# Kernel tuning notes

Hardware: AMD Instinct MI355X
Metric: run time of the kernel (lower is better)

The kernel has to match this reference:

```python
import jax, jax.numpy as jnp
import numpy as np

INVALID_VALUE = 0.0
FIX_SEARCH_AREA = 1  # search window half-width -> (2s+1)^2 candidates


def setup_inputs() -> dict:
    key = jax.random.key(0)
    k1, k2, k3 = jax.random.split(key, 3)
    B, C, H, W = 8, 1, 512, 512
    Ho, Wo = 1024, 1024
    depth = jax.random.uniform(k1, (B, C, H, W), dtype=jnp.float32, minval=0.5, maxval=5.0)
    holes = jax.random.uniform(k2, (B, C, H, W)) < 0.25
    depth = jnp.where(holes, INVALID_VALUE, depth)
    # normalized grid coords in [-1.2, 1.2]: some samples out of bounds (Zeros padding)
    grid = jax.random.uniform(k3, (B, Ho, Wo, 2), dtype=jnp.float32, minval=-1.2, maxval=1.2)
    return {"input": depth, "grid": grid}


def _search_offsets(s):
    # center offset first, then ring offsets in row-major order
    offs = [(0, 0)] + [(dy, dx) for dy in range(-s, s + 1) for dx in range(-s, s + 1)
                       if not (dy == 0 and dx == 0)]
    dys = jnp.array([o[0] for o in offs], dtype=jnp.int32)
    dxs = jnp.array([o[1] for o in offs], dtype=jnp.int32)
    return dys, dxs


def reference(input, grid):
    """MaskPlusFix nearest sampling with local search-area fix, Zeros padding,
    align_corners=True. input: (B,C,H,W), grid: (B,Ho,Wo,2) -> (B,C,Ho,Wo)."""
    B, C, H, W = input.shape
    # unnormalize (align_corners=True): [-1,1] -> [0, size-1]
    x = (grid[..., 0] + 1.0) * 0.5 * (W - 1)
    y = (grid[..., 1] + 1.0) * 0.5 * (H - 1)
    ix = jnp.round(x).astype(jnp.int32)  # nearest pixel (B,Ho,Wo)
    iy = jnp.round(y).astype(jnp.int32)

    dys, dxs = _search_offsets(FIX_SEARCH_AREA)  # (K,)
    cix = ix[..., None] + dxs  # (B,Ho,Wo,K)
    ciy = iy[..., None] + dys
    inb = (cix >= 0) & (cix < W) & (ciy >= 0) & (ciy < H)  # Zeros padding: OOB invalid
    cixc = jnp.clip(cix, 0, W - 1)
    ciyc = jnp.clip(ciy, 0, H - 1)

    # gather candidates: (B,C,Ho,Wo,K)
    vals = jax.vmap(lambda img, yy, xx: img[:, yy, xx])(input, ciyc, cixc)
    valid = inb[:, None] & (vals != INVALID_VALUE)
    first = jnp.argmax(valid, axis=-1)
    any_valid = jnp.any(valid, axis=-1)
    sel = jnp.take_along_axis(vals, first[..., None], axis=-1)[..., 0]
    return jnp.where(any_valid, sel, INVALID_VALUE)
```

## Files before the change

kernel.cpp:

```cpp
#include <hip/hip_runtime.h>


#define SC_B  8
#define SC_H  512
#define SC_W  512
#define SC_HO 1024
#define SC_WO 1024

__global__ __launch_bounds__(256) void SpaceCarverGridSamplerModule_kernel(
    const float* __restrict__ depth,
    const float* __restrict__ grid,
    float* __restrict__ out,
    int total)
{
    int idx = blockIdx.x * blockDim.x + threadIdx.x;
    if (idx >= total) return;

    int b = idx >> 20;

    float2 g = reinterpret_cast<const float2*>(grid)[idx];

    float x = (g.x + 1.0f) * 0.5f * (float)(SC_W - 1);
    float y = (g.y + 1.0f) * 0.5f * (float)(SC_H - 1);

    int ix = (int)rintf(x);
    int iy = (int)rintf(y);

    const float* __restrict__ img = depth + (size_t)b * (SC_H * SC_W);

    const int dys[9] = { 0, -1, -1, -1,  0, 0,  1, 1, 1 };
    const int dxs[9] = { 0, -1,  0,  1, -1, 1, -1, 0, 1 };

    float result = 0.0f;
    #pragma unroll
    for (int k = 0; k < 9; ++k) {
        int cy = iy + dys[k];
        int cx = ix + dxs[k];
        if (cy >= 0 && cy < SC_H && cx >= 0 && cx < SC_W) {
            float v = img[cy * SC_W + cx];
            if (v != 0.0f) { result = v; break; }
        }
    }

    out[idx] = result;
}

extern "C" void kernel_launch(void* const* d_in, const int* in_sizes, int n_in,
                              void* d_out, int out_size, void* d_ws, size_t ws_size,
                              hipStream_t stream) {
    const float* depth = (const float*)d_in[0];
    const float* grid  = (const float*)d_in[1];
    float* out = (float*)d_out;

    int total = out_size;
    dim3 block(256);
    dim3 gridDim((total + block.x - 1) / block.x);
    SpaceCarverGridSamplerModule_kernel<<<gridDim, block, 0, stream>>>(depth, grid, out, total);
}
```

Baseline: 144.6 us.

## Process two samples per thread and issue all nine gathers unconditionally

```diff
diff --git a/kernel.cpp b/kernel.cpp
--- a/kernel.cpp
+++ b/kernel.cpp
@@ -7,42 +7,59 @@
 #define SC_HO 1024
 #define SC_WO 1024
 
+__device__ __forceinline__ float sample_one(const float* __restrict__ img,
+                                            float gx, float gy)
+{
+    float x = (gx + 1.0f) * 0.5f * (float)(SC_W - 1);
+    float y = (gy + 1.0f) * 0.5f * (float)(SC_H - 1);
+
+    int ix = (int)rintf(x);
+    int iy = (int)rintf(y);
+
+    const int dys[9] = { 0, -1, -1, -1,  0, 0,  1, 1, 1 };
+    const int dxs[9] = { 0, -1,  0,  1, -1, 1, -1, 0, 1 };
+
+    float v[9];
+    bool  inb[9];
+    #pragma unroll
+    for (int k = 0; k < 9; ++k) {
+        int cy = iy + dys[k];
+        int cx = ix + dxs[k];
+        inb[k] = (cy >= 0) & (cy < SC_H) & (cx >= 0) & (cx < SC_W);
+        int cyc = min(max(cy, 0), SC_H - 1);
+        int cxc = min(max(cx, 0), SC_W - 1);
+        v[k] = img[cyc * SC_W + cxc];
+    }
+
+    float result = 0.0f;
+    #pragma unroll
+    for (int k = 8; k >= 0; --k) {
+        bool valid = inb[k] & (v[k] != 0.0f);
+        result = valid ? v[k] : result;
+    }
+    return result;
+}
+
 __global__ __launch_bounds__(256) void SpaceCarverGridSamplerModule_kernel(
     const float* __restrict__ depth,
     const float* __restrict__ grid,
     float* __restrict__ out,
-    int total)
+    int total_pairs)
 {
-    int idx = blockIdx.x * blockDim.x + threadIdx.x;
-    if (idx >= total) return;
+    int t = blockIdx.x * blockDim.x + threadIdx.x;
+    if (t >= total_pairs) return;
 
-    int b = idx >> 20;
+    int idx0 = t * 2;
+    int b = idx0 >> 20;
 
-    float2 g = reinterpret_cast<const float2*>(grid)[idx];
-
-    float x = (g.x + 1.0f) * 0.5f * (float)(SC_W - 1);
-    float y = (g.y + 1.0f) * 0.5f * (float)(SC_H - 1);
-
-    int ix = (int)rintf(x);
-    int iy = (int)rintf(y);
+    float4 g = reinterpret_cast<const float4*>(grid)[t];
 
     const float* __restrict__ img = depth + (size_t)b * (SC_H * SC_W);
 
-    const int dys[9] = { 0, -1, -1, -1,  0, 0,  1, 1, 1 };
-    const int dxs[9] = { 0, -1,  0,  1, -1, 1, -1, 0, 1 };
+    float r0 = sample_one(img, g.x, g.y);
+    float r1 = sample_one(img, g.z, g.w);
 
-    float result = 0.0f;
-    #pragma unroll
-    for (int k = 0; k < 9; ++k) {
-        int cy = iy + dys[k];
-        int cx = ix + dxs[k];
-        if (cy >= 0 && cy < SC_H && cx >= 0 && cx < SC_W) {
-            float v = img[cy * SC_W + cx];
-            if (v != 0.0f) { result = v; break; }
-        }
-    }
-
-    out[idx] = result;
+    reinterpret_cast<float2*>(out)[t] = make_float2(r0, r1);
 }
 
 extern "C" void kernel_launch(void* const* d_in, const int* in_sizes, int n_in,
@@ -52,8 +69,8 @@
     const float* grid  = (const float*)d_in[1];
     float* out = (float*)d_out;
 
-    int total = out_size;
+    int total_pairs = out_size / 2;
     dim3 block(256);
-    dim3 gridDim((total + block.x - 1) / block.x);
-    SpaceCarverGridSamplerModule_kernel<<<gridDim, block, 0, stream>>>(depth, grid, out, total);
+    dim3 gridDim((total_pairs + block.x - 1) / block.x);
+    SpaceCarverGridSamplerModule_kernel<<<gridDim, block, 0, stream>>>(depth, grid, out, total_pairs);
 }
```

After: 219.0 us. 51.4% more time.

## Precompute fixed depth map in padded buffer, then single-gather sampling

Applied to the files above, without the earlier changes.

```diff
diff --git a/kernel.cpp b/kernel.cpp
--- a/kernel.cpp
+++ b/kernel.cpp
@@ -7,7 +7,92 @@
 #define SC_HO 1024
 #define SC_WO 1024
 
-__global__ __launch_bounds__(256) void SpaceCarverGridSamplerModule_kernel(
+#define FP_H  514
+#define FP_W  514
+#define FP_S  516
+#define FP_BATCH (FP_H * FP_S)
+
+__global__ __launch_bounds__(256) void build_fixed_kernel(
+    const float* __restrict__ depth,
+    float* __restrict__ fixedPad)
+{
+    int b = blockIdx.y;
+    int t = blockIdx.x * blockDim.x + threadIdx.x;
+    if (t >= FP_H * FP_W) return;
+    int py = t / FP_W;
+    int px = t - py * FP_W;
+    int y = py - 1;
+    int x = px - 1;
+
+    const float* __restrict__ img = depth + (size_t)b * (SC_H * SC_W);
+
+    const int dys[9] = { 0, -1, -1, -1,  0, 0,  1, 1, 1 };
+    const int dxs[9] = { 0, -1,  0,  1, -1, 1, -1, 0, 1 };
+
+    float v[9];
+    bool  inb[9];
+    #pragma unroll
+    for (int k = 0; k < 9; ++k) {
+        int cy = y + dys[k];
+        int cx = x + dxs[k];
+        inb[k] = (cy >= 0) & (cy < SC_H) & (cx >= 0) & (cx < SC_W);
+        int cyc = min(max(cy, 0), SC_H - 1);
+        int cxc = min(max(cx, 0), SC_W - 1);
+        v[k] = img[cyc * SC_W + cxc];
+    }
+
+    float result = 0.0f;
+    #pragma unroll
+    for (int k = 8; k >= 0; --k) {
+        bool valid = inb[k] & (v[k] != 0.0f);
+        result = valid ? v[k] : result;
+    }
+
+    fixedPad[(size_t)b * FP_BATCH + py * FP_S + px] = result;
+}
+
+__device__ __forceinline__ float sample_fixed(const float* __restrict__ fp,
+                                              float gx, float gy)
+{
+    float x = (gx + 1.0f) * 0.5f * (float)(SC_W - 1);
+    float y = (gy + 1.0f) * 0.5f * (float)(SC_H - 1);
+    int ix = (int)rintf(x);
+    int iy = (int)rintf(y);
+
+    bool inrange = (ix >= -1) & (ix <= SC_W) & (iy >= -1) & (iy <= SC_H);
+    int px = min(max(ix + 1, 0), FP_W - 1);
+    int py = min(max(iy + 1, 0), FP_H - 1);
+    float v = fp[py * FP_S + px];
+    return inrange ? v : 0.0f;
+}
+
+__global__ __launch_bounds__(256) void sample_kernel(
+    const float* __restrict__ fixedPad,
+    const float* __restrict__ grid,
+    float* __restrict__ out,
+    int total_quads)
+{
+    int t = blockIdx.x * blockDim.x + threadIdx.x;
+    if (t >= total_quads) return;
+
+    int p0 = t * 4;
+    int b = p0 >> 20;
+
+    const float4* g4 = reinterpret_cast<const float4*>(grid);
+    float4 gA = g4[2 * t];
+    float4 gB = g4[2 * t + 1];
+
+    const float* __restrict__ fp = fixedPad + (size_t)b * FP_BATCH;
+
+    float r0 = sample_fixed(fp, gA.x, gA.y);
+    float r1 = sample_fixed(fp, gA.z, gA.w);
+    float r2 = sample_fixed(fp, gB.x, gB.y);
+    float r3 = sample_fixed(fp, gB.z, gB.w);
+
+    reinterpret_cast<float4*>(out)[t] = make_float4(r0, r1, r2, r3);
+}
+
+__global__ __launch_bounds__(256) void fallback_kernel(
     const float* __restrict__ depth,
     const float* __restrict__ grid,
     float* __restrict__ out,
@@ -15,22 +100,15 @@
 {
     int idx = blockIdx.x * blockDim.x + threadIdx.x;
     if (idx >= total) return;
-
     int b = idx >> 20;
-
     float2 g = reinterpret_cast<const float2*>(grid)[idx];
-
     float x = (g.x + 1.0f) * 0.5f * (float)(SC_W - 1);
     float y = (g.y + 1.0f) * 0.5f * (float)(SC_H - 1);
-
     int ix = (int)rintf(x);
     int iy = (int)rintf(y);
-
     const float* __restrict__ img = depth + (size_t)b * (SC_H * SC_W);
-
     const int dys[9] = { 0, -1, -1, -1,  0, 0,  1, 1, 1 };
     const int dxs[9] = { 0, -1,  0,  1, -1, 1, -1, 0, 1 };
-
     float result = 0.0f;
     #pragma unroll
     for (int k = 0; k < 9; ++k) {
@@ -41,7 +119,6 @@
             if (v != 0.0f) { result = v; break; }
         }
     }
-
     out[idx] = result;
 }
 
@@ -52,8 +129,23 @@
     const float* grid  = (const float*)d_in[1];
     float* out = (float*)d_out;
 
-    int total = out_size;
-    dim3 block(256);
-    dim3 gridDim((total + block.x - 1) / block.x);
-    SpaceCarverGridSamplerModule_kernel<<<gridDim, block, 0, stream>>>(depth, grid, out, total);
+    size_t need = (size_t)SC_B * FP_BATCH * sizeof(float);
+    if (ws_size >= need) {
+        float* fixedPad = (float*)d_ws;
+
+        int per_batch = FP_H * FP_W;
+        dim3 b1(256);
+        dim3 g1((per_batch + b1.x - 1) / b1.x, SC_B);
+        build_fixed_kernel<<<g1, b1, 0, stream>>>(depth, fixedPad);
+
+        int total_quads = out_size / 4;
+        dim3 b2(256);
+        dim3 g2((total_quads + b2.x - 1) / b2.x);
+        sample_kernel<<<g2, b2, 0, stream>>>(fixedPad, grid, out, total_quads);
+    } else {
+        int total = out_size;
+        dim3 block(256);
+        dim3 gridDim((total + block.x - 1) / block.x);
+        fallback_kernel<<<gridDim, block, 0, stream>>>(depth, grid, out, total);
+    }
 }
```

Result: no change. 145.2 us (+0.4%).
